# Kernel optimization log

Hardware: AMD Instinct MI355X
Metric: run time of the kernel (lower is better)

## Reference

```python
import jax, jax.numpy as jnp
import numpy as np

D_MODEL = 512
EXPAND = 2
D_INNER = EXPAND * D_MODEL          # 1024
HEADDIM = 64
NHEADS = D_INNER // HEADDIM         # 16
D_STATE = 64
NGROUPS = 1
D_CONV = 7
D_FF = 2048
CONV_DIM = D_INNER + 2 * NGROUPS * D_STATE              # 1152
D_IN_PROJ = 2 * D_INNER + 2 * NGROUPS * D_STATE + 2 * NHEADS  # 2208
BATCH, SEQLEN = 4, 2048
EPS = 1e-5


def setup_inputs() -> dict:
    key = jax.random.key(0)
    ks = jax.random.split(key, 8)
    g = lambda k, shape, scale: jax.random.normal(k, shape, jnp.float32) * scale
    # dt_bias = inverse softplus of dt values in [1e-3, 0.1] (Mamba2 init convention)
    dt = jnp.linspace(1e-3, 0.1, NHEADS, dtype=jnp.float32)
    return {
        "x": jax.random.normal(ks[0], (BATCH, SEQLEN, D_MODEL), jnp.float32),
        "ln1_w": jnp.ones((D_MODEL,), jnp.float32),
        "ln1_b": jnp.zeros((D_MODEL,), jnp.float32),
        "in_proj_w": g(ks[1], (D_IN_PROJ, D_MODEL), 0.02),
        "conv_w": g(ks[2], (CONV_DIM, D_CONV), 0.2),
        "conv_b": jnp.zeros((CONV_DIM,), jnp.float32),
        "dt_bias": jnp.log(jnp.expm1(dt)),
        "A_log": jnp.log(jnp.arange(1, NHEADS + 1, dtype=jnp.float32)),
        "Dp": jnp.ones((NHEADS,), jnp.float32),
        "rms_w": jnp.ones((D_INNER,), jnp.float32),
        "out_proj_w": g(ks[3], (D_MODEL, D_INNER), 0.02),
        "ln2_w": jnp.ones((D_MODEL,), jnp.float32),
        "ln2_b": jnp.zeros((D_MODEL,), jnp.float32),
        "fc1_w": g(ks[4], (D_FF, D_MODEL), 0.02),
        "fc1_b": jnp.zeros((D_FF,), jnp.float32),
        "fc2_w": g(ks[5], (D_MODEL, D_FF), 0.02),
        "fc2_b": jnp.zeros((D_MODEL,), jnp.float32),
    }


def _layernorm(x, w, b):
    mu = jnp.mean(x, -1, keepdims=True)
    var = jnp.mean((x - mu) ** 2, -1, keepdims=True)
    return (x - mu) * jax.lax.rsqrt(var + EPS) * w + b


def _hydra(u, in_proj_w, conv_w, conv_b, dt_bias, A_log, Dp, rms_w, out_proj_w):
    B, L, _ = u.shape
    zxbcdt = u @ in_proj_w.T                                   # (B,L,D_IN_PROJ)
    z = zxbcdt[..., :D_INNER]                                  # gate
    xBC = zxbcdt[..., D_INNER:D_INNER + CONV_DIM]
    dt = zxbcdt[..., D_INNER + CONV_DIM:]                      # (B,L,2H)
    # forward / (time-reversed) backward dt, stacked on batch dim -> (2B,L,H)
    dt = jnp.concatenate([dt[..., :NHEADS], jnp.flip(dt[..., NHEADS:], axis=1)], axis=0)
    dt = jax.nn.softplus(dt + dt_bias)
    # depthwise causal conv1d (torch padding=d_conv-1 then [:, :L])
    xc = jax.lax.conv_general_dilated(
        jnp.transpose(xBC, (0, 2, 1)), conv_w[:, None, :],
        window_strides=(1,), padding=[(D_CONV - 1, 0)],
        feature_group_count=CONV_DIM, dimension_numbers=("NCH", "OIH", "NCH"))
    xBC = jax.nn.silu(jnp.transpose(xc, (0, 2, 1)) + conv_b)   # (B,L,CONV_DIM)
    xs = xBC[..., :D_INNER]
    Bm = xBC[..., D_INNER:D_INNER + NGROUPS * D_STATE]
    Cm = xBC[..., D_INNER + NGROUPS * D_STATE:]
    x_og = xs
    both = lambda a: jnp.concatenate([a, jnp.flip(a, axis=1)], axis=0)  # (2B,...)
    xs, Bm, Cm = both(xs), both(Bm), both(Cm)
    xh = xs.reshape(2 * B, L, NHEADS, HEADDIM)
    A = -jnp.exp(A_log)                                        # (H,) scalar-per-head SSD
    decay = jnp.exp(A * dt)                                    # (2B,L,H)
    dtx = dt[..., None] * xh                                   # (2B,L,H,P)

    def step(h, inp):
        dec_t, dtx_t, B_t, C_t = inp
        # h: (2B,H,P,N)
        h = h * dec_t[..., None, None] + dtx_t[..., None] * B_t[:, None, None, :]
        y = jnp.einsum("bhpn,bn->bhp", h, C_t)
        return h, y

    h0 = jnp.zeros((2 * B, NHEADS, HEADDIM, D_STATE), u.dtype)
    mv = lambda a: jnp.moveaxis(a, 1, 0)  # time-major for scan
    _, y = jax.lax.scan(step, h0, (mv(decay), mv(dtx), mv(Bm), mv(Cm)))
    y = jnp.moveaxis(y, 0, 1).reshape(2 * B, L, D_INNER)
    # shift by one (strictly off-diagonal quasiseparable parts)
    y = jnp.concatenate([jnp.zeros_like(y[:, :1]), y[:, :-1]], axis=1)
    y_fw, y_bw = y[:B], jnp.flip(y[B:], axis=1)
    y = y_fw + y_bw + x_og * jnp.repeat(Dp, HEADDIM)           # diagonal via D
    # gated RMSNorm then out projection
    yg = y * jax.nn.silu(z)
    yg = yg * jax.lax.rsqrt(jnp.mean(yg * yg, -1, keepdims=True) + EPS) * rms_w
    return yg @ out_proj_w.T


def reference(x, ln1_w, ln1_b, in_proj_w, conv_w, conv_b, dt_bias, A_log, Dp,
              rms_w, out_proj_w, ln2_w, ln2_b, fc1_w, fc1_b, fc2_w, fc2_b):
    # pre-norm Hydra block with residual (dropout = identity at eval)
    h = _layernorm(x, ln1_w, ln1_b)
    x = x + _hydra(h, in_proj_w, conv_w, conv_b, dt_bias, A_log, Dp, rms_w, out_proj_w)
    # FFN block with its own pre-norm + residual
    f = _layernorm(x, ln2_w, ln2_b)
    f = jax.nn.gelu(f @ fc1_w.T + fc1_b, approximate=False)
    f = f @ fc2_w.T + fc2_b
    return x + f
```

## Files before the change

kernel.cpp:

```cpp
#include <hip/hip_runtime.h>
#include <math.h>

#define D_MODEL   512
#define D_INNER   1024
#define NHEADS    16
#define HEADDIM   64
#define D_STATE   64
#define D_CONV    7
#define D_FF      2048
#define CONV_DIM  1152
#define D_IN_PROJ 2208
#define BATCH     4
#define SEQLEN    2048
#define NTOK      (BATCH*SEQLEN)
#define EPS       1e-5f

#define OFF_XBCB  9043968ull
#define OFF_XT    13762560ull
#define OFF_YFW   17956864ull
#define OFF_YBW   26345472ull
#define OFF_SREG  34734080ull

typedef __bf16 bf16x8 __attribute__((ext_vector_type(8)));
typedef float  f32x4  __attribute__((ext_vector_type(4)));

__device__ __forceinline__ float siluf(float x) { return x / (1.f + expf(-x)); }
__device__ __forceinline__ float geluf(float x) { return 0.5f * x * (1.f + erff(x * 0.70710678118654752f)); }
__device__ __forceinline__ float softplusf(float x) { return fmaxf(x, 0.f) + log1pf(expf(-fabsf(x))); }
__device__ __forceinline__ int tglob(int d, int c, int t) { int s = c * 64 + t; return d ? (SEQLEN - 1 - s) : s; }
__device__ __forceinline__ unsigned short f2bf(float f) {
    unsigned int u = __float_as_uint(f);
    u += 0x7FFFu + ((u >> 16) & 1u);
    return (unsigned short)(u >> 16);
}
__device__ __forceinline__ float bf2f(unsigned short u) { return __uint_as_float((unsigned)u << 16); }
__device__ __forceinline__ void glds16(const void* g, void* l) {
    __builtin_amdgcn_global_load_lds((const __attribute__((address_space(1))) void*)g,
                                     (__attribute__((address_space(3))) void*)l, 16, 0, 0);
}

__global__ __launch_bounds__(256) void ln_kernel(const float* __restrict__ x,
                                                 const float* __restrict__ w,
                                                 const float* __restrict__ b,
                                                 unsigned short* __restrict__ out, int nrows)
{
    int wid = threadIdx.x >> 6;
    int lane = threadIdx.x & 63;
    int row = blockIdx.x * 4 + wid;
    if (row >= nrows) return;
    const float* xr = x + (size_t)row * D_MODEL;
    float4 v0 = *(const float4*)(xr + lane * 8);
    float4 v1 = *(const float4*)(xr + lane * 8 + 4);
    float v[8] = {v0.x, v0.y, v0.z, v0.w, v1.x, v1.y, v1.z, v1.w};
    float s = 0.f;
#pragma unroll
    for (int i = 0; i < 8; i++) s += v[i];
#pragma unroll
    for (int m = 1; m < 64; m <<= 1) s += __shfl_xor(s, m, 64);
    float mu = s * (1.f / D_MODEL);
    float q = 0.f;
#pragma unroll
    for (int i = 0; i < 8; i++) { float dd = v[i] - mu; q += dd * dd; }
#pragma unroll
    for (int m = 1; m < 64; m <<= 1) q += __shfl_xor(q, m, 64);
    float inv = rsqrtf(q * (1.f / D_MODEL) + EPS);
    float4 w0 = *(const float4*)(w + lane * 8);
    float4 w1 = *(const float4*)(w + lane * 8 + 4);
    float4 b0 = *(const float4*)(b + lane * 8);
    float4 b1 = *(const float4*)(b + lane * 8 + 4);
    float o[8];
    o[0] = (v[0]-mu)*inv*w0.x + b0.x; o[1] = (v[1]-mu)*inv*w0.y + b0.y;
    o[2] = (v[2]-mu)*inv*w0.z + b0.z; o[3] = (v[3]-mu)*inv*w0.w + b0.w;
    o[4] = (v[4]-mu)*inv*w1.x + b1.x; o[5] = (v[5]-mu)*inv*w1.y + b1.y;
    o[6] = (v[6]-mu)*inv*w1.z + b1.z; o[7] = (v[7]-mu)*inv*w1.w + b1.w;
    unsigned short* orow = out + (size_t)row * D_MODEL + lane * 8;
    ushort4 p0, p1;
    p0.x = f2bf(o[0]); p0.y = f2bf(o[1]); p0.z = f2bf(o[2]); p0.w = f2bf(o[3]);
    p1.x = f2bf(o[4]); p1.y = f2bf(o[5]); p1.z = f2bf(o[6]); p1.w = f2bf(o[7]);
    *(ushort4*)orow = p0;
    *(ushort4*)(orow + 4) = p1;
}

__global__ __launch_bounds__(256) void wconv_all(const float* __restrict__ w0, unsigned short* __restrict__ p0,
                                                 const float* __restrict__ w1, unsigned short* __restrict__ p1,
                                                 const float* __restrict__ w2, unsigned short* __restrict__ p2,
                                                 const float* __restrict__ w3, unsigned short* __restrict__ p3)
{
    int i = blockIdx.x * 256 + threadIdx.x;
    const float* src; unsigned short* dst; int srcn;
    if (i < 294912)      { src = w0; dst = p0; srcn = 282624; }
    else if (i < 425984) { i -= 294912; src = w1; dst = p1; srcn = 131072; }
    else if (i < 688128) { i -= 425984; src = w2; dst = p2; srcn = 262144; }
    else                 { i -= 688128; src = w3; dst = p3; srcn = 262144; }
    ushort4 o = make_ushort4(0, 0, 0, 0);
    if (i < srcn) {
        float4 v = ((const float4*)src)[i];
        o.x = f2bf(v.x); o.y = f2bf(v.y); o.z = f2bf(v.z); o.w = f2bf(v.w);
    }
    ((ushort4*)dst)[i] = o;
}

__global__ __launch_bounds__(256, 2) void gemm_bf16(const unsigned short* __restrict__ A,
                                                    const unsigned short* __restrict__ W,
                                                    int K, int Nreal,
                                                    float* __restrict__ Cf,
                                                    unsigned short* __restrict__ Cb,
                                                    const float* __restrict__ bias,
                                                    const float* __restrict__ res, int act,
                                                    float* __restrict__ dtf)
{
    __shared__ unsigned short As[2][128 * 32];
    __shared__ unsigned short Ws[2][128 * 32];
    const int tid = threadIdx.x;
    const int wave = tid >> 6;
    const int lane = tid & 63;
    const int m0 = blockIdx.x * 128;
    const int n0 = blockIdx.y * 128;
    const int wm = (wave & 1) * 64;
    const int wn = (wave >> 1) * 64;

    const size_t gA = (size_t)(m0 + 32 * wave + (lane >> 2)) * K + (lane & 3) * 8;
    const size_t gW = (size_t)(n0 + 32 * wave + (lane >> 2)) * K + (lane & 3) * 8;
    const int lofs = wave * 1024 + lane * 8;

    const int fr = lane & 15;
    const int fq = (lane >> 4) * 8;
    f32x4 acc[4][4] = {};

    for (int k0 = 0; k0 < K; k0 += 64) {
        glds16(A + gA + k0, As[0] + lofs);
        glds16(A + gA + (size_t)16 * K + k0, As[0] + lofs + 512);
        glds16(A + gA + k0 + 32, As[1] + lofs);
        glds16(A + gA + (size_t)16 * K + k0 + 32, As[1] + lofs + 512);
        glds16(W + gW + k0, Ws[0] + lofs);
        glds16(W + gW + (size_t)16 * K + k0, Ws[0] + lofs + 512);
        glds16(W + gW + k0 + 32, Ws[1] + lofs);
        glds16(W + gW + (size_t)16 * K + k0 + 32, Ws[1] + lofs + 512);
        __syncthreads();
#pragma unroll
        for (int p = 0; p < 2; p++) {
            bf16x8 af[4], bf[4];
#pragma unroll
            for (int mi = 0; mi < 4; mi++)
                af[mi] = *(const bf16x8*)(As[p] + (wm + mi * 16 + fr) * 32 + fq);
#pragma unroll
            for (int ni = 0; ni < 4; ni++)
                bf[ni] = *(const bf16x8*)(Ws[p] + (wn + ni * 16 + fr) * 32 + fq);
#pragma unroll
            for (int mi = 0; mi < 4; mi++)
#pragma unroll
                for (int ni = 0; ni < 4; ni++)
                    acc[mi][ni] = __builtin_amdgcn_mfma_f32_16x16x32_bf16(af[mi], bf[ni], acc[mi][ni], 0, 0, 0);
        }
        __syncthreads();
    }

    const int colb = n0 + wn + (lane & 15);
    const int rowb = m0 + wm + (lane >> 4) * 4;
#pragma unroll
    for (int mi = 0; mi < 4; mi++) {
#pragma unroll
        for (int ni = 0; ni < 4; ni++) {
            int col = colb + ni * 16;
            if (col < Nreal) {
#pragma unroll
                for (int r = 0; r < 4; r++) {
                    int row = rowb + mi * 16 + r;
                    float v = acc[mi][ni][r];
                    size_t idx = (size_t)row * Nreal + col;
                    if (bias) v += bias[col];
                    if (res) v += res[idx];
                    if (act) v = geluf(v);
                    if (Cb) {
                        Cb[idx] = f2bf(v);
                        if (dtf && col >= 2176) dtf[(size_t)row * 32 + (col - 2176)] = v;
                    } else Cf[idx] = v;
                }
            }
        }
    }
}

__global__ __launch_bounds__(256) void gemm_bf16_t64(const unsigned short* __restrict__ A,
                                                     const unsigned short* __restrict__ W,
                                                     int K, int N,
                                                     float* __restrict__ Cf,
                                                     const float* __restrict__ bias,
                                                     const float* __restrict__ res)
{
    __shared__ unsigned short As[2][64 * 32];
    __shared__ unsigned short Ws[2][64 * 32];
    const int tid = threadIdx.x;
    const int wave = tid >> 6;
    const int lane = tid & 63;
    const int m0 = blockIdx.x * 64;
    const int n0 = blockIdx.y * 64;

    const size_t gA = (size_t)(m0 + (tid >> 2)) * K + (tid & 3) * 8;
    const size_t gW = (size_t)(n0 + (tid >> 2)) * K + (tid & 3) * 8;
    const int lofs = tid * 8;

    const int fr = lane & 15;
    const int fq = (lane >> 4) * 8;
    f32x4 acc[4] = {};

    for (int k0 = 0; k0 < K; k0 += 64) {
        glds16(A + gA + k0, As[0] + lofs);
        glds16(A + gA + k0 + 32, As[1] + lofs);
        glds16(W + gW + k0, Ws[0] + lofs);
        glds16(W + gW + k0 + 32, Ws[1] + lofs);
        __syncthreads();
#pragma unroll
        for (int p = 0; p < 2; p++) {
            bf16x8 af = *(const bf16x8*)(As[p] + (wave * 16 + fr) * 32 + fq);
#pragma unroll
            for (int ni = 0; ni < 4; ni++) {
                bf16x8 bfr = *(const bf16x8*)(Ws[p] + (ni * 16 + fr) * 32 + fq);
                acc[ni] = __builtin_amdgcn_mfma_f32_16x16x32_bf16(af, bfr, acc[ni], 0, 0, 0);
            }
        }
        __syncthreads();
    }

    const int col0 = n0 + (lane & 15);
    const int rowb = m0 + wave * 16 + (lane >> 4) * 4;
#pragma unroll
    for (int ni = 0; ni < 4; ni++) {
        int col = col0 + ni * 16;
        float bb = bias ? bias[col] : 0.f;
#pragma unroll
        for (int r = 0; r < 4; r++) {
            int row = rowb + r;
            size_t idx = (size_t)row * N + col;
            float v = acc[ni][r] + bb;
            if (res) v += res[idx];
            Cf[idx] = v;
        }
    }
}

__global__ __launch_bounds__(256) void conv_kernel(const unsigned short* __restrict__ zx,
                                                   const float* __restrict__ conv_w,
                                                   const float* __restrict__ conv_b,
                                                   unsigned short* __restrict__ out)
{
    int gid = blockIdx.x * 256 + threadIdx.x;
    int c4 = gid % 288;
    int tt = gid / 288;
    int c = c4 * 4;
    int b = tt >> 8;
    int t0 = (tt & 255) * 8;

    float wgt[4][7], bias[4];
#pragma unroll
    for (int q = 0; q < 4; q++) {
        bias[q] = conv_b[c + q];
#pragma unroll
        for (int j = 0; j < 7; j++) wgt[q][j] = conv_w[(c + q) * 7 + j];
    }

    float xin[4][14];
    const unsigned short* base = zx + (size_t)(b * SEQLEN + t0) * D_IN_PROJ + D_INNER + c;
#pragma unroll
    for (int j = 0; j < 14; j++) {
        int t = t0 - 6 + j;
        ushort4 v = make_ushort4(0, 0, 0, 0);
        if (t >= 0) v = *(const ushort4*)(base + (ptrdiff_t)(j - 6) * D_IN_PROJ);
        xin[0][j] = bf2f(v.x); xin[1][j] = bf2f(v.y);
        xin[2][j] = bf2f(v.z); xin[3][j] = bf2f(v.w);
    }

    unsigned short* orow = out + (size_t)(b * SEQLEN + t0) * CONV_DIM + c;
#pragma unroll
    for (int i = 0; i < 8; i++) {
        ushort4 o;
        float a0 = bias[0], a1 = bias[1], a2 = bias[2], a3 = bias[3];
#pragma unroll
        for (int j = 0; j < 7; j++) {
            a0 = fmaf(wgt[0][j], xin[0][i + j], a0);
            a1 = fmaf(wgt[1][j], xin[1][i + j], a1);
            a2 = fmaf(wgt[2][j], xin[2][i + j], a2);
            a3 = fmaf(wgt[3][j], xin[3][i + j], a3);
        }
        o.x = f2bf(siluf(a0)); o.y = f2bf(siluf(a1));
        o.z = f2bf(siluf(a2)); o.w = f2bf(siluf(a3));
        *(ushort4*)(orow + (size_t)i * CONV_DIM) = o;
    }
}

__global__ __launch_bounds__(256) void xpose_kernel(const unsigned short* __restrict__ xbc,
                                                    unsigned short* __restrict__ xT)
{
    int tt = blockIdx.x, pt = blockIdx.y, b = blockIdx.z;
    __shared__ unsigned short T[64][68];
    {
        int r = threadIdx.x >> 4, q = threadIdx.x & 15;
#pragma unroll
        for (int i = 0; i < 4; i++) {
            int t = tt * 64 + r + i * 16;
            ushort4 v = *(const ushort4*)(xbc + (size_t)(b * SEQLEN + t) * CONV_DIM + pt * 64 + q * 4);
            *(ushort4*)&T[r + i * 16][q * 4] = v;
        }
    }
    __syncthreads();
    {
        int p = threadIdx.x >> 4, tq = threadIdx.x & 15;
#pragma unroll
        for (int i = 0; i < 4; i++) {
            int pp = p + i * 16;
            ushort4 o;
            o.x = T[tq * 4 + 0][pp]; o.y = T[tq * 4 + 1][pp];
            o.z = T[tq * 4 + 2][pp]; o.w = T[tq * 4 + 3][pp];
            *(ushort4*)(xT + ((size_t)b * 1024 + pt * 64 + pp) * 2048 + tt * 64 + tq * 4) = o;
        }
    }
}

__global__ __launch_bounds__(256) void dt_table_kernel(const float* __restrict__ dtf,
                                                       const float* __restrict__ dt_bias,
                                                       const float* __restrict__ A_log,
                                                       float* __restrict__ cum_tab,
                                                       float* __restrict__ dtv_tab)
{
    int wid = blockIdx.x * 4 + (threadIdx.x >> 6);
    int lane = threadIdx.x & 63;
    int c = wid & 31, h = (wid >> 5) & 15, b = (wid >> 9) & 3, d = wid >> 11;
    int tg = tglob(d, c, lane);
    float raw = dtf[(size_t)(b * SEQLEN + tg) * 32 + d * 16 + h] + dt_bias[h];
    float dtv = softplusf(raw);
    float cum = -expf(A_log[h]) * dtv;
#pragma unroll
    for (int off = 1; off < 64; off <<= 1) {
        int src = lane - off;
        float o = __shfl(cum, src < 0 ? 0 : src, 64);
        if (lane >= off) cum += o;
    }
    cum_tab[(size_t)wid * 64 + lane] = cum;
    dtv_tab[(size_t)wid * 64 + lane] = dtv;
}

__global__ __launch_bounds__(256) void ssd_intra_mfma(const unsigned short* __restrict__ xbc,
                                                      const unsigned short* __restrict__ xT,
                                                      const float* __restrict__ cum_tab,
                                                      const float* __restrict__ dtv_tab,
                                                      float* __restrict__ y_fw,
                                                      float* __restrict__ y_bw)
{
    const int bid = blockIdx.x;
    const int hq = bid & 3, c = (bid >> 2) & 31, b = (bid >> 7) & 3, d = bid >> 9;
    const int tid = threadIdx.x, wave = tid >> 6, lane = tid & 63;

    __shared__ unsigned short BnMt[64 * 80];
    __shared__ unsigned short CnXt[64 * 80];
    __shared__ float Gm[64 * 68];
    __shared__ float cum_l[64], dtv_l[64];

    if (c == 0) {
        int t0 = d ? (SEQLEN - 1) : 0;
        float* ybuf = d ? y_bw : y_fw;
        ybuf[(size_t)(b * SEQLEN + t0) * D_INNER + hq * 256 + tid] = 0.f;
    }
    {
        int s = tid >> 2, nq = (tid & 3) * 16;
        int tg = tglob(d, c, s);
        const unsigned short* row = xbc + (size_t)(b * SEQLEN + tg) * CONV_DIM;
#pragma unroll
        for (int k = 0; k < 16; k += 4) {
            *(ushort4*)&BnMt[s * 80 + nq + k] = *(const ushort4*)(row + 1024 + nq + k);
            *(ushort4*)&CnXt[s * 80 + nq + k] = *(const ushort4*)(row + 1088 + nq + k);
        }
    }
    __syncthreads();
    {
        f32x4 ga[4] = {};
        const int mrow = wave * 16 + (lane & 15);
        const int kq = (lane >> 4) * 8;
#pragma unroll
        for (int k0 = 0; k0 < 64; k0 += 32) {
            bf16x8 afr = *(const bf16x8*)&BnMt[mrow * 80 + k0 + kq];
#pragma unroll
            for (int ni = 0; ni < 4; ni++) {
                bf16x8 bfr = *(const bf16x8*)&CnXt[(ni * 16 + (lane & 15)) * 80 + k0 + kq];
                ga[ni] = __builtin_amdgcn_mfma_f32_16x16x32_bf16(afr, bfr, ga[ni], 0, 0, 0);
            }
        }
        int col = lane & 15, quad = lane >> 4;
#pragma unroll
        for (int ni = 0; ni < 4; ni++)
#pragma unroll
            for (int r = 0; r < 4; r++)
                Gm[(wave * 16 + quad * 4 + r) * 68 + ni * 16 + col] = ga[ni][r];
    }

    for (int hh = 0; hh < 4; hh++) {
        const int h = hq * 4 + hh;
        __syncthreads();
        if (tid < 64) {
            int flat = ((d * 4 + b) * 16 + h) * 32 + c;
            cum_l[tid] = cum_tab[(size_t)flat * 64 + tid];
            dtv_l[tid] = dtv_tab[(size_t)flat * 64 + tid];
        }
        {
            const unsigned short* xrow = xT + ((size_t)b * 1024 + h * 64) * 2048;
            int p = tid >> 4, tq = tid & 15;
#pragma unroll
            for (int pi = 0; pi < 4; pi++, p += 16) {
                if (d == 0) {
                    ushort4 v = *(const ushort4*)(xrow + (size_t)p * 2048 + c * 64 + tq * 4);
                    *(ushort4*)&CnXt[p * 80 + tq * 4] = v;
                } else {
                    int base = SEQLEN - 64 - c * 64;
                    ushort4 v = *(const ushort4*)(xrow + (size_t)p * 2048 + base + (15 - tq) * 4);
                    CnXt[p * 80 + tq * 4 + 0] = v.w;
                    CnXt[p * 80 + tq * 4 + 1] = v.z;
                    CnXt[p * 80 + tq * 4 + 2] = v.y;
                    CnXt[p * 80 + tq * 4 + 3] = v.x;
                }
            }
        }
        __syncthreads();
        {
            int s = tid & 63, tq = tid >> 6;
            float cs = cum_l[s], dv = dtv_l[s];
#pragma unroll
            for (int j = 0; j < 16; j++) {
                int t = tq * 16 + j;
                float g = Gm[s * 68 + t];
                float m = (s <= t) ? g * expf(cum_l[t] - cs) * dv : 0.f;
                BnMt[t * 80 + s] = f2bf(m);
            }
        }
        __syncthreads();
        {
            f32x4 acc[4] = {};
            const int mrow = wave * 16 + (lane & 15);
            const int kq = (lane >> 4) * 8;
#pragma unroll
            for (int k0 = 0; k0 < 64; k0 += 32) {
                bf16x8 afr = *(const bf16x8*)&BnMt[mrow * 80 + k0 + kq];
#pragma unroll
                for (int ni = 0; ni < 4; ni++) {
                    bf16x8 bfr = *(const bf16x8*)&CnXt[(ni * 16 + (lane & 15)) * 80 + k0 + kq];
                    acc[ni] = __builtin_amdgcn_mfma_f32_16x16x32_bf16(afr, bfr, acc[ni], 0, 0, 0);
                }
            }
            float* ybuf = d ? y_bw : y_fw;
            int quad = lane >> 4, col0 = lane & 15;
#pragma unroll
            for (int r = 0; r < 4; r++) {
                int tl = wave * 16 + quad * 4 + r;
                int tg = tglob(d, c, tl);
                int tout = d ? (tg - 1) : (tg + 1);
                if (tout >= 0 && tout < SEQLEN) {
                    float* yp = ybuf + (size_t)(b * SEQLEN + tout) * D_INNER + h * 64;
#pragma unroll
                    for (int ni = 0; ni < 4; ni++)
                        yp[ni * 16 + col0] = acc[ni][r];
                }
            }
        }
    }
}

__global__ __launch_bounds__(256) void ssd_state_kernel(const unsigned short* __restrict__ xbc,
                                                        const float* __restrict__ cum_tab,
                                                        const float* __restrict__ dtv_tab,
                                                        unsigned short* __restrict__ sreg16)
{
    const int flat = blockIdx.x;
    const int c = flat & 31, h = (flat >> 5) & 15, b = (flat >> 9) & 3, d = flat >> 11;
    const int tid = threadIdx.x;
    const int ty = tid >> 4, tx = tid & 15;

    __shared__ float Bm[64][64];
    __shared__ float Xw[64][64];
    __shared__ float cum_l[64], dtv_l[64];

    if (tid < 64) {
        cum_l[tid] = cum_tab[(size_t)flat * 64 + tid];
        dtv_l[tid] = dtv_tab[(size_t)flat * 64 + tid];
    }
    __syncthreads();
    float clast = cum_l[63];
    for (int idx = tid; idx < 1024; idx += 256) {
        int s = idx >> 4, q = idx & 15;
        int tg = tglob(d, c, s);
        const unsigned short* row = xbc + (size_t)(b * SEQLEN + tg) * CONV_DIM;
        ushort4 ub = *(const ushort4*)(row + 1024 + q * 4);
        ushort4 ux = *(const ushort4*)(row + h * 64 + q * 4);
        float w = expf(clast - cum_l[s]) * dtv_l[s];
        Bm[s][q*4+0] = bf2f(ub.x); Bm[s][q*4+1] = bf2f(ub.y);
        Bm[s][q*4+2] = bf2f(ub.z); Bm[s][q*4+3] = bf2f(ub.w);
        Xw[s][q*4+0] = bf2f(ux.x)*w; Xw[s][q*4+1] = bf2f(ux.y)*w;
        Xw[s][q*4+2] = bf2f(ux.z)*w; Xw[s][q*4+3] = bf2f(ux.w)*w;
    }
    __syncthreads();
    float acc[4][4] = {};
    for (int s = 0; s < 64; s++) {
        float4 xv = *(const float4*)&Xw[s][ty * 4];
        float4 bv = *(const float4*)&Bm[s][tx * 4];
        float xx[4] = {xv.x, xv.y, xv.z, xv.w};
        float bb[4] = {bv.x, bv.y, bv.z, bv.w};
#pragma unroll
        for (int i = 0; i < 4; i++)
#pragma unroll
            for (int j = 0; j < 4; j++) acc[i][j] = fmaf(xx[i], bb[j], acc[i][j]);
    }
    unsigned short* st = sreg16 + (size_t)flat * 4096;
#pragma unroll
    for (int i = 0; i < 4; i++) {
        ushort4 o;
        o.x = f2bf(acc[i][0]); o.y = f2bf(acc[i][1]);
        o.z = f2bf(acc[i][2]); o.w = f2bf(acc[i][3]);
        *(ushort4*)&st[(size_t)(ty * 4 + i) * 64 + tx * 4] = o;
    }
}

__global__ __launch_bounds__(256) void ssd_chunkscan_kernel(const float* __restrict__ cum_tab,
                                                            unsigned short* __restrict__ sreg16)
{
    const int ps = blockIdx.x & 3;
    const int g  = blockIdx.x >> 2;
    const int tid = threadIdx.x;
    const int base = g * 32;
    const size_t off = (size_t)ps * 1024 + tid * 4;
    float h0 = 0.f, h1 = 0.f, h2 = 0.f, h3 = 0.f;
    ushort4 s = *(ushort4*)(sreg16 + (size_t)base * 4096 + off);
    for (int c = 0; c < 32; c++) {
        int flat = base + c;
        ushort4 snext;
        if (c < 31) snext = *(ushort4*)(sreg16 + (size_t)(flat + 1) * 4096 + off);
        float dec = expf(cum_tab[(size_t)flat * 64 + 63]);
        ushort4 o;
        o.x = f2bf(h0); o.y = f2bf(h1); o.z = f2bf(h2); o.w = f2bf(h3);
        *(ushort4*)(sreg16 + (size_t)flat * 4096 + off) = o;
        h0 = h0 * dec + bf2f(s.x);
        h1 = h1 * dec + bf2f(s.y);
        h2 = h2 * dec + bf2f(s.z);
        h3 = h3 * dec + bf2f(s.w);
        s = snext;
    }
}

__global__ __launch_bounds__(256) void ssd_inter_mfma(const unsigned short* __restrict__ xbc,
                                                      const float* __restrict__ cum_tab,
                                                      const unsigned short* __restrict__ sreg16,
                                                      float* __restrict__ y_fw,
                                                      float* __restrict__ y_bw)
{
    const int flat = blockIdx.x;
    const int c = flat & 31;
    if (c == 0) return;
    const int h = (flat >> 5) & 15, b = (flat >> 9) & 3, d = flat >> 11;
    const int tid = threadIdx.x, wave = tid >> 6, lane = tid & 63;

    __shared__ unsigned short Cs[64 * 72];
    __shared__ unsigned short Hs[64 * 72];
    __shared__ float cum_l[64];

    if (tid < 64) cum_l[tid] = cum_tab[(size_t)flat * 64 + tid];
    {
        int s = tid >> 2, nq = (tid & 3) * 16;
        int tg = tglob(d, c, s);
        const unsigned short* row = xbc + (size_t)(b * SEQLEN + tg) * CONV_DIM + 1088;
        const unsigned short* st = sreg16 + (size_t)flat * 4096 + s * 64;
#pragma unroll
        for (int k = 0; k < 16; k += 4) {
            *(ushort4*)&Cs[s * 72 + nq + k] = *(const ushort4*)(row + nq + k);
            *(ushort4*)&Hs[s * 72 + nq + k] = *(const ushort4*)(st + nq + k);
        }
    }
    __syncthreads();
    f32x4 acc[4] = {};
    const int fr = lane & 15, kq = (lane >> 4) * 8;
    const int mrow = wave * 16 + fr;
#pragma unroll
    for (int k0 = 0; k0 < 64; k0 += 32) {
        bf16x8 afr = *(const bf16x8*)&Cs[mrow * 72 + k0 + kq];
#pragma unroll
        for (int ni = 0; ni < 4; ni++) {
            bf16x8 bfr = *(const bf16x8*)&Hs[(ni * 16 + fr) * 72 + k0 + kq];
            acc[ni] = __builtin_amdgcn_mfma_f32_16x16x32_bf16(afr, bfr, acc[ni], 0, 0, 0);
        }
    }
    float* ybuf = d ? y_bw : y_fw;
    int quad = lane >> 4, col0 = lane & 15;
#pragma unroll
    for (int r = 0; r < 4; r++) {
        int tl = wave * 16 + quad * 4 + r;
        float a = expf(cum_l[tl]);
        int tg = tglob(d, c, tl);
        int tout = d ? (tg - 1) : (tg + 1);
        if (tout >= 0 && tout < SEQLEN) {
            float* yp = ybuf + (size_t)(b * SEQLEN + tout) * D_INNER + h * 64;
#pragma unroll
            for (int ni = 0; ni < 4; ni++)
                yp[ni * 16 + col0] += acc[ni][r] * a;
        }
    }
}

__global__ __launch_bounds__(256) void combine_kernel(const unsigned short* __restrict__ zx,
                                                      const unsigned short* __restrict__ xbc,
                                                      const float* __restrict__ y_fw,
                                                      const float* __restrict__ y_bw,
                                                      const float* __restrict__ Dp,
                                                      const float* __restrict__ rms_w,
                                                      unsigned short* __restrict__ yg)
{
    int row = blockIdx.x;
    int i = threadIdx.x * 4;
    float4 yf = *(const float4*)(y_fw + (size_t)row * D_INNER + i);
    float4 yb = *(const float4*)(y_bw + (size_t)row * D_INNER + i);
    ushort4 uxs = *(const ushort4*)(xbc + (size_t)row * CONV_DIM + i);
    ushort4 uz  = *(const ushort4*)(zx + (size_t)row * D_IN_PROJ + i);
    float dp = Dp[i >> 6];
    float g[4];
    g[0] = (yf.x + yb.x + bf2f(uxs.x) * dp) * siluf(bf2f(uz.x));
    g[1] = (yf.y + yb.y + bf2f(uxs.y) * dp) * siluf(bf2f(uz.y));
    g[2] = (yf.z + yb.z + bf2f(uxs.z) * dp) * siluf(bf2f(uz.z));
    g[3] = (yf.w + yb.w + bf2f(uxs.w) * dp) * siluf(bf2f(uz.w));
    float ss = g[0]*g[0] + g[1]*g[1] + g[2]*g[2] + g[3]*g[3];
#pragma unroll
    for (int m = 1; m < 64; m <<= 1) ss += __shfl_xor(ss, m, 64);
    __shared__ float red[4];
    if ((threadIdx.x & 63) == 0) red[threadIdx.x >> 6] = ss;
    __syncthreads();
    ss = red[0] + red[1] + red[2] + red[3];
    float scale = rsqrtf(ss * (1.f / D_INNER) + EPS);
    float4 rw = *(const float4*)(rms_w + i);
    ushort4 o;
    o.x = f2bf(g[0] * scale * rw.x); o.y = f2bf(g[1] * scale * rw.y);
    o.z = f2bf(g[2] * scale * rw.z); o.w = f2bf(g[3] * scale * rw.w);
    *(ushort4*)(yg + (size_t)row * D_INNER + i) = o;
}

extern "C" void kernel_launch(void* const* d_in, const int* in_sizes, int n_in,
                              void* d_out, int out_size, void* d_ws, size_t ws_size,
                              hipStream_t stream)
{
    const float* x         = (const float*)d_in[0];
    const float* ln1_w     = (const float*)d_in[1];
    const float* ln1_b     = (const float*)d_in[2];
    const float* in_proj_w = (const float*)d_in[3];
    const float* conv_w    = (const float*)d_in[4];
    const float* conv_b    = (const float*)d_in[5];
    const float* dt_bias   = (const float*)d_in[6];
    const float* A_log     = (const float*)d_in[7];
    const float* Dp        = (const float*)d_in[8];
    const float* rms_w     = (const float*)d_in[9];
    const float* out_proj_w= (const float*)d_in[10];
    const float* ln2_w     = (const float*)d_in[11];
    const float* ln2_b     = (const float*)d_in[12];
    const float* fc1_w     = (const float*)d_in[13];
    const float* fc1_b     = (const float*)d_in[14];
    const float* fc2_w     = (const float*)d_in[15];
    const float* fc2_b     = (const float*)d_in[16];
    float* out = (float*)d_out;

    float* ws0 = (float*)d_ws;
    unsigned short* zx_bf  = (unsigned short*)ws0;
    unsigned short* xbc_bf = (unsigned short*)(ws0 + OFF_XBCB);
    unsigned short* xT_bf  = (unsigned short*)(ws0 + OFF_XT);
    float* y_fw = ws0 + OFF_YFW;
    float* y_bw = ws0 + OFF_YBW;
    float* sreg = ws0 + OFF_SREG;
    unsigned short* sreg16 = (unsigned short*)sreg;
    unsigned short* hA_bf = (unsigned short*)sreg;
    unsigned short* yg_bf = (unsigned short*)(sreg + 2686976);
    float* x_res          = sreg + 6881280;
    unsigned short* sh    = (unsigned short*)sreg;
    unsigned short* P_in  = sh + 22151168;
    unsigned short* P_out = sh + 23330816;
    unsigned short* P_f1  = sh + 23855104;
    unsigned short* P_f2  = sh + 24903680;
    unsigned short* f1_bf = (unsigned short*)ws0;
    float* cum_tab = out;
    float* dtv_tab = out + 262144;
    float* dtf     = out + 524288;

    wconv_all<<<dim3(3712), dim3(256), 0, stream>>>(in_proj_w, P_in, out_proj_w, P_out, fc1_w, P_f1, fc2_w, P_f2);
    ln_kernel<<<dim3(NTOK / 4), dim3(256), 0, stream>>>(x, ln1_w, ln1_b, hA_bf, NTOK);
    gemm_bf16<<<dim3(64, 18), dim3(256), 0, stream>>>(hA_bf, P_in, 512, 2208, nullptr, zx_bf, nullptr, nullptr, 0, dtf);
    conv_kernel<<<dim3(288 * 1024 / 256), dim3(256), 0, stream>>>(zx_bf, conv_w, conv_b, xbc_bf);
    xpose_kernel<<<dim3(32, 16, 4), dim3(256), 0, stream>>>(xbc_bf, xT_bf);
    dt_table_kernel<<<dim3(1024), dim3(256), 0, stream>>>(dtf, dt_bias, A_log, cum_tab, dtv_tab);
    ssd_intra_mfma<<<dim3(1024), dim3(256), 0, stream>>>(xbc_bf, xT_bf, cum_tab, dtv_tab, y_fw, y_bw);
    ssd_state_kernel<<<dim3(4096), dim3(256), 0, stream>>>(xbc_bf, cum_tab, dtv_tab, sreg16);
    ssd_chunkscan_kernel<<<dim3(512), dim3(256), 0, stream>>>(cum_tab, sreg16);
    ssd_inter_mfma<<<dim3(4096), dim3(256), 0, stream>>>(xbc_bf, cum_tab, sreg16, y_fw, y_bw);
    combine_kernel<<<dim3(NTOK), dim3(256), 0, stream>>>(zx_bf, xbc_bf, y_fw, y_bw, Dp, rms_w, yg_bf);
    gemm_bf16_t64<<<dim3(128, 8), dim3(256), 0, stream>>>(yg_bf, P_out, 1024, 512, x_res, nullptr, x);
    ln_kernel<<<dim3(NTOK / 4), dim3(256), 0, stream>>>(x_res, ln2_w, ln2_b, hA_bf, NTOK);
    gemm_bf16<<<dim3(64, 16), dim3(256), 0, stream>>>(hA_bf, P_f1, 512, 2048, nullptr, f1_bf, fc1_b, nullptr, 1, nullptr);
    gemm_bf16_t64<<<dim3(128, 8), dim3(256), 0, stream>>>(f1_bf, P_f2, 2048, 512, out, fc2_b, x_res);
}
```

Measured before the change: 397.6 us.

## Swizzle GEMM LDS layout and move SSD chunk-state computation to MFMA

Adds an XOR swizzle on the k-chunk index for both GEMM kernels' global-to-LDS loads and fragment reads, to cut LDS bank conflicts when reading MFMA fragments. Also rewrites the SSD chunk-state kernel to use bf16 MFMA instead of scalar fp32 FMAs. The decay-weighted X comes from the transposed xT buffer and B is staged transposed in padded LDS. The weighted X is now rounded to bf16 before the product, which adds some precision loss.

Measured after the change: 379.7 us. 1.05x faster.

```diff
diff --git a/kernel.cpp b/kernel.cpp
--- a/kernel.cpp
+++ b/kernel.cpp
@@ -119,12 +119,13 @@
     const int wm = (wave & 1) * 64;
     const int wn = (wave >> 1) * 64;
 
-    const size_t gA = (size_t)(m0 + 32 * wave + (lane >> 2)) * K + (lane & 3) * 8;
-    const size_t gW = (size_t)(n0 + 32 * wave + (lane >> 2)) * K + (lane & 3) * 8;
+    const int kchunk = ((lane & 3) ^ ((lane >> 3) & 3)) * 8;
+    const size_t gA = (size_t)(m0 + 32 * wave + (lane >> 2)) * K + kchunk;
+    const size_t gW = (size_t)(n0 + 32 * wave + (lane >> 2)) * K + kchunk;
     const int lofs = wave * 1024 + lane * 8;
 
     const int fr = lane & 15;
-    const int fq = (lane >> 4) * 8;
+    const int fq = ((lane >> 4) ^ ((fr >> 1) & 3)) * 8;
     f32x4 acc[4][4] = {};
 
     for (int k0 = 0; k0 < K; k0 += 64) {
@@ -196,12 +197,13 @@
     const int m0 = blockIdx.x * 64;
     const int n0 = blockIdx.y * 64;
 
-    const size_t gA = (size_t)(m0 + (tid >> 2)) * K + (tid & 3) * 8;
-    const size_t gW = (size_t)(n0 + (tid >> 2)) * K + (tid & 3) * 8;
+    const int kchunk = ((tid & 3) ^ ((tid >> 3) & 3)) * 8;
+    const size_t gA = (size_t)(m0 + (tid >> 2)) * K + kchunk;
+    const size_t gW = (size_t)(n0 + (tid >> 2)) * K + kchunk;
     const int lofs = tid * 8;
 
     const int fr = lane & 15;
-    const int fq = (lane >> 4) * 8;
+    const int fq = ((lane >> 4) ^ ((fr >> 1) & 3)) * 8;
     f32x4 acc[4] = {};
 
     for (int k0 = 0; k0 < K; k0 += 64) {
@@ -462,57 +464,80 @@
     }
 }
 
-__global__ __launch_bounds__(256) void ssd_state_kernel(const unsigned short* __restrict__ xbc,
-                                                        const float* __restrict__ cum_tab,
-                                                        const float* __restrict__ dtv_tab,
-                                                        unsigned short* __restrict__ sreg16)
+__global__ __launch_bounds__(256) void ssd_state_mfma(const unsigned short* __restrict__ xbc,
+                                                      const unsigned short* __restrict__ xT,
+                                                      const float* __restrict__ cum_tab,
+                                                      const float* __restrict__ dtv_tab,
+                                                      unsigned short* __restrict__ sreg16)
 {
     const int flat = blockIdx.x;
     const int c = flat & 31, h = (flat >> 5) & 15, b = (flat >> 9) & 3, d = flat >> 11;
-    const int tid = threadIdx.x;
-    const int ty = tid >> 4, tx = tid & 15;
-
-    __shared__ float Bm[64][64];
-    __shared__ float Xw[64][64];
+    const int tid = threadIdx.x, wave = tid >> 6, lane = tid & 63;
+
+    __shared__ unsigned short Xs[64 * 72];
+    __shared__ unsigned short Bs[64 * 72];
     __shared__ float cum_l[64], dtv_l[64];
 
     if (tid < 64) {
         cum_l[tid] = cum_tab[(size_t)flat * 64 + tid];
         dtv_l[tid] = dtv_tab[(size_t)flat * 64 + tid];
     }
+    {
+        int s = tid >> 2, nq = (tid & 3) * 16;
+        int tg = tglob(d, c, s);
+        const unsigned short* row = xbc + (size_t)(b * SEQLEN + tg) * CONV_DIM + 1024;
+#pragma unroll
+        for (int k = 0; k < 16; k += 4) {
+            ushort4 vb = *(const ushort4*)(row + nq + k);
+            Bs[(nq + k + 0) * 72 + s] = vb.x;
+            Bs[(nq + k + 1) * 72 + s] = vb.y;
+            Bs[(nq + k + 2) * 72 + s] = vb.z;
+            Bs[(nq + k + 3) * 72 + s] = vb.w;
+        }
+    }
     __syncthreads();
-    float clast = cum_l[63];
-    for (int idx = tid; idx < 1024; idx += 256) {
-        int s = idx >> 4, q = idx & 15;
-        int tg = tglob(d, c, s);
-        const unsigned short* row = xbc + (size_t)(b * SEQLEN + tg) * CONV_DIM;
-        ushort4 ub = *(const ushort4*)(row + 1024 + q * 4);
-        ushort4 ux = *(const ushort4*)(row + h * 64 + q * 4);
-        float w = expf(clast - cum_l[s]) * dtv_l[s];
-        Bm[s][q*4+0] = bf2f(ub.x); Bm[s][q*4+1] = bf2f(ub.y);
-        Bm[s][q*4+2] = bf2f(ub.z); Bm[s][q*4+3] = bf2f(ub.w);
-        Xw[s][q*4+0] = bf2f(ux.x)*w; Xw[s][q*4+1] = bf2f(ux.y)*w;
-        Xw[s][q*4+2] = bf2f(ux.z)*w; Xw[s][q*4+3] = bf2f(ux.w)*w;
+    {
+        const float clast = cum_l[63];
+        const unsigned short* xrow = xT + ((size_t)b * 1024 + h * 64) * 2048;
+        int p = tid >> 4, tq = tid & 15;
+#pragma unroll
+        for (int pi = 0; pi < 4; pi++, p += 16) {
+            ushort4 v;
+            if (d == 0) {
+                v = *(const ushort4*)(xrow + (size_t)p * 2048 + c * 64 + tq * 4);
+            } else {
+                int base = SEQLEN - 64 - c * 64;
+                ushort4 t = *(const ushort4*)(xrow + (size_t)p * 2048 + base + (15 - tq) * 4);
+                v.x = t.w; v.y = t.z; v.z = t.y; v.w = t.x;
+            }
+            int s0 = tq * 4;
+            Xs[p * 72 + s0 + 0] = f2bf(bf2f(v.x) * expf(clast - cum_l[s0 + 0]) * dtv_l[s0 + 0]);
+            Xs[p * 72 + s0 + 1] = f2bf(bf2f(v.y) * expf(clast - cum_l[s0 + 1]) * dtv_l[s0 + 1]);
+            Xs[p * 72 + s0 + 2] = f2bf(bf2f(v.z) * expf(clast - cum_l[s0 + 2]) * dtv_l[s0 + 2]);
+            Xs[p * 72 + s0 + 3] = f2bf(bf2f(v.w) * expf(clast - cum_l[s0 + 3]) * dtv_l[s0 + 3]);
+        }
     }
     __syncthreads();
-    float acc[4][4] = {};
-    for (int s = 0; s < 64; s++) {
-        float4 xv = *(const float4*)&Xw[s][ty * 4];
-        float4 bv = *(const float4*)&Bm[s][tx * 4];
-        float xx[4] = {xv.x, xv.y, xv.z, xv.w};
-        float bb[4] = {bv.x, bv.y, bv.z, bv.w};
-#pragma unroll
-        for (int i = 0; i < 4; i++)
-#pragma unroll
-            for (int j = 0; j < 4; j++) acc[i][j] = fmaf(xx[i], bb[j], acc[i][j]);
+    f32x4 acc[4] = {};
+    const int fr = lane & 15, kq = (lane >> 4) * 8;
+    const int mrow = wave * 16 + fr;
+#pragma unroll
+    for (int k0 = 0; k0 < 64; k0 += 32) {
+        bf16x8 afr = *(const bf16x8*)&Xs[mrow * 72 + k0 + kq];
+#pragma unroll
+        for (int ni = 0; ni < 4; ni++) {
+            bf16x8 bfr = *(const bf16x8*)&Bs[(ni * 16 + fr) * 72 + k0 + kq];
+            acc[ni] = __builtin_amdgcn_mfma_f32_16x16x32_bf16(afr, bfr, acc[ni], 0, 0, 0);
+        }
     }
     unsigned short* st = sreg16 + (size_t)flat * 4096;
-#pragma unroll
-    for (int i = 0; i < 4; i++) {
-        ushort4 o;
-        o.x = f2bf(acc[i][0]); o.y = f2bf(acc[i][1]);
-        o.z = f2bf(acc[i][2]); o.w = f2bf(acc[i][3]);
-        *(ushort4*)&st[(size_t)(ty * 4 + i) * 64 + tx * 4] = o;
+    int quad = lane >> 4, col0 = lane & 15;
+#pragma unroll
+    for (int r = 0; r < 4; r++) {
+        int p = wave * 16 + quad * 4 + r;
+#pragma unroll
+        for (int ni = 0; ni < 4; ni++)
+            st[(size_t)p * 64 + ni * 16 + col0] = f2bf(acc[ni][r]);
     }
 }
 
@@ -686,7 +711,7 @@
     xpose_kernel<<<dim3(32, 16, 4), dim3(256), 0, stream>>>(xbc_bf, xT_bf);
     dt_table_kernel<<<dim3(1024), dim3(256), 0, stream>>>(dtf, dt_bias, A_log, cum_tab, dtv_tab);
     ssd_intra_mfma<<<dim3(1024), dim3(256), 0, stream>>>(xbc_bf, xT_bf, cum_tab, dtv_tab, y_fw, y_bw);
-    ssd_state_kernel<<<dim3(4096), dim3(256), 0, stream>>>(xbc_bf, cum_tab, dtv_tab, sreg16);
+    ssd_state_mfma<<<dim3(4096), dim3(256), 0, stream>>>(xbc_bf, xT_bf, cum_tab, dtv_tab, sreg16);
     ssd_chunkscan_kernel<<<dim3(512), dim3(256), 0, stream>>>(cum_tab, sreg16);
     ssd_inter_mfma<<<dim3(4096), dim3(256), 0, stream>>>(xbc_bf, cum_tab, sreg16, y_fw, y_bw);
     combine_kernel<<<dim3(NTOK), dim3(256), 0, stream>>>(zx_bf, xbc_bf, y_fw, y_bw, Dp, rms_w, yg_bf);
```
